# Performance work log

Hardware: AMD Instinct MI355X
Metric: run time of the kernel (lower is better)

## Reference

```python
import jax, jax.numpy as jnp
import numpy as np

B_SI = 4.1491   # neutron scattering length Si (fm)
B_O = 5.803     # neutron scattering length O (fm)
CUTOFF = 3.5    # tetrahedral neighbour cutoff (A)
BIG = 1e6       # masked-distance sentinel (finite to keep grads NaN-free)


def setup_inputs() -> dict:
    key = jax.random.key(0)
    k1, k2 = jax.random.split(key)
    N, L = 4096, 40.0
    positions = jax.random.uniform(k1, (N, 3), dtype=jnp.float32) * L
    cell = (L * jnp.eye(3)).astype(jnp.float32)
    r_bins = (0.05 + 0.05 * jnp.arange(200, dtype=jnp.float32))      # 0.05..10.0 A
    q_bins = jnp.linspace(0.5, 25.0, 500, dtype=jnp.float32)          # A^-1
    species = jax.random.randint(k2, (N,), 0, 3, dtype=jnp.int32)     # 0=Si, 1/2=O
    return {"positions": positions, "cell": cell, "r_bins": r_bins,
            "q_bins": q_bins, "species": species}


def _pair_geometry(positions, cell):
    # Minimum-image displacements under a general periodic cell.
    disp = positions[:, None, :] - positions[None, :, :]        # [N,N,3]
    frac = disp @ jnp.linalg.inv(cell)
    frac = frac - jnp.round(frac)
    disp = frac @ cell
    d2 = jnp.sum(disp * disp, axis=-1)                           # [N,N]
    self_mask = jnp.eye(positions.shape[0], dtype=bool)
    dist = jnp.sqrt(jnp.where(self_mask, 1.0, d2))               # safe sqrt on diag
    return disp, dist, self_mask


def reference(positions, cell, r_bins, q_bins, species):
    N = positions.shape[0]
    nbins = r_bins.shape[0]
    dtype = positions.dtype

    disp, dist, self_mask = _pair_geometry(positions, cell)

    # --- neutron-weighted G(r): differentiable linear (cloud-in-cell) binning ---
    b = jnp.where(species == 0, B_SI, B_O).astype(dtype)         # per-atom scattering length
    w = (b[:, None] * b[None, :]) / (jnp.mean(b) ** 2)           # Faber-Ziman pair weights
    r0, dr = r_bins[0], r_bins[1] - r_bins[0]
    x = (dist - r0) / dr
    i0 = jnp.floor(x).astype(jnp.int32)
    f = x - i0.astype(dtype)
    valid = (~self_mask) & (i0 >= 0) & (i0 < nbins - 1)
    w0 = jnp.where(valid, w * (1.0 - f), 0.0).ravel()
    w1 = jnp.where(valid, w * f, 0.0).ravel()
    i0f = jnp.clip(i0, 0, nbins - 1).ravel()
    hist = (jnp.zeros(nbins, dtype)
            .at[i0f].add(w0)
            .at[jnp.clip(i0f + 1, 0, nbins - 1)].add(w1))
    V = jnp.abs(jnp.linalg.det(cell))
    rho = N / V
    shell = 4.0 * jnp.pi * r_bins ** 2 * dr                       # ideal-gas shell volume
    G_r = hist / (N * rho * shell)                                # [nbins]

    # --- total correlation function T(r) = 4 pi rho r G(r) ---
    T_r = 4.0 * jnp.pi * rho * r_bins * G_r

    # --- structure factor S(Q) = 1 + 4 pi rho int r^2 (G(r)-1) sinc(Qr) dr ---
    qr = q_bins[:, None] * r_bins[None, :]                        # [nQ, nr]
    integrand = (r_bins ** 2) * (G_r - 1.0)
    S_Q = 1.0 + 4.0 * jnp.pi * rho * dr * jnp.sum(
        integrand[None, :] * jnp.sinc(qr / jnp.pi), axis=1)

    # --- tetrahedral order parameter q_tet over Si centres with O neighbours ---
    central = species == 0
    nbr_ok = (species != 0)[None, :] & (~self_mask)
    nd = jnp.where(nbr_ok, dist, BIG)
    negd, idx = jax.lax.top_k(-nd, 4)                             # 4 nearest O per atom
    d4 = -negd                                                    # [N,4]
    u = jnp.take_along_axis(disp, idx[:, :, None], axis=1) / d4[:, :, None]  # unit vecs
    cosang = jnp.einsum('nkd,nld->nkl', u, u)                     # [N,4,4]
    pair_mask = jnp.triu(jnp.ones((4, 4), bool), 1)               # 6 angle pairs
    q_i = 1.0 - (3.0 / 8.0) * jnp.sum(((cosang + 1.0 / 3.0) ** 2) * pair_mask, axis=(1, 2))
    vf = (central & (d4[:, 3] < CUTOFF)).astype(dtype)            # needs 4 nbrs in cutoff
    q_tet = jnp.sum(q_i * vf) / jnp.maximum(jnp.sum(vf), 1.0)

    return G_r, T_r, S_Q, q_tet
```

## Files before the change

kernel.cpp:

```cpp
#include <hip/hip_runtime.h>
#include <climits>
#include <math.h>


#define B_SI_F 4.1491f
#define B_O_F  5.803f
#define CUTOFF_F 3.5f
#define CS2 12.25350025f
#define NCOPIES 16
#define CAP 32

#define WS_HIST 16
#define WS_CNT  4096

__device__ __forceinline__ bool dless(float da, int ia, float db, int ib) {
    return (da < db) || (da == db && ia < ib);
}

struct CellK {
    float ci0, ci1, ci2, ci3, ci4, ci5, ci6, ci7, ci8;
    float c0, c1, c2, c3, c4, c5, c6, c7, c8;
};

__device__ __forceinline__ CellK make_cell(const float* __restrict__ cellm,
                                           bool& diag) {
    CellK K;
    K.c0 = cellm[0]; K.c1 = cellm[1]; K.c2 = cellm[2];
    K.c3 = cellm[3]; K.c4 = cellm[4]; K.c5 = cellm[5];
    K.c6 = cellm[6]; K.c7 = cellm[7]; K.c8 = cellm[8];
    double m0 = K.c0, m1 = K.c1, m2 = K.c2;
    double m3 = K.c3, m4 = K.c4, m5 = K.c5;
    double m6 = K.c6, m7 = K.c7, m8 = K.c8;
    double det = m0*(m4*m8 - m5*m7) - m1*(m3*m8 - m5*m6) + m2*(m3*m7 - m4*m6);
    double rd = 1.0 / det;
    K.ci0 = (float)( (m4*m8 - m5*m7) * rd);
    K.ci1 = (float)(-(m1*m8 - m2*m7) * rd);
    K.ci2 = (float)( (m1*m5 - m2*m4) * rd);
    K.ci3 = (float)(-(m3*m8 - m5*m6) * rd);
    K.ci4 = (float)( (m0*m8 - m2*m6) * rd);
    K.ci5 = (float)(-(m0*m5 - m2*m3) * rd);
    K.ci6 = (float)( (m3*m7 - m4*m6) * rd);
    K.ci7 = (float)(-(m0*m7 - m1*m6) * rd);
    K.ci8 = (float)( (m0*m4 - m1*m3) * rd);
    diag = (K.c1 == 0.0f) && (K.c2 == 0.0f) && (K.c3 == 0.0f) &&
           (K.c5 == 0.0f) && (K.c6 == 0.0f) && (K.c7 == 0.0f);
    return K;
}

template<bool DIAG>
__device__ __forceinline__ void min_image(const CellK& K,
                                          float dx, float dy, float dz,
                                          float& ex, float& ey, float& ez) {
    if (DIAG) {
        float t0 = dx * K.ci0, t1 = dy * K.ci4, t2 = dz * K.ci8;
        t0 -= rintf(t0);  t1 -= rintf(t1);  t2 -= rintf(t2);
        ex = t0 * K.c0;  ey = t1 * K.c4;  ez = t2 * K.c8;
    } else {
        float f0 = dx*K.ci0 + dy*K.ci3 + dz*K.ci6;
        float f1 = dx*K.ci1 + dy*K.ci4 + dz*K.ci7;
        float f2 = dx*K.ci2 + dy*K.ci5 + dz*K.ci8;
        f0 -= rintf(f0);  f1 -= rintf(f1);  f2 -= rintf(f2);
        ex = f0*K.c0 + f1*K.c3 + f2*K.c6;
        ey = f0*K.c1 + f1*K.c4 + f2*K.c7;
        ez = f0*K.c2 + f1*K.c5 + f2*K.c8;
    }
}

template<bool DIAG>
__device__ __forceinline__ void hist_sweep(const CellK& K,
                                           const float4* __restrict__ sj,
                                           const float4* __restrict__ sjc,
                                           int lbase, int jb0,
                                           float fi0, float fi1, float fi2,
                                           float xi, float yi, float zi,
                                           float wi, float inv_dr, float nrb0,
                                           int nbins_m1, float* shc,
                                           bool iSi, bool iO, bool offdiag, int iidx,
                                           float* __restrict__ cnt,
                                           float4* __restrict__ cand) {
    #pragma unroll 4
    for (int l = 0; l < 64; ++l) {
        const float4 pj = sj[lbase + l];
        float d0 = fi0 - pj.x;  d0 -= rintf(d0);
        float d1 = fi1 - pj.y;  d1 -= rintf(d1);
        float d2 = fi2 - pj.z;  d2 -= rintf(d2);
        float ex, ey, ez;
        if (DIAG) {
            ex = d0 * K.c0;  ey = d1 * K.c4;  ez = d2 * K.c8;
        } else {
            ex = d0*K.c0 + d1*K.c3 + d2*K.c6;
            ey = d0*K.c1 + d1*K.c4 + d2*K.c7;
            ez = d0*K.c2 + d1*K.c5 + d2*K.c8;
        }
        float dsq  = fmaf(ex, ex, fmaf(ey, ey, ez * ez));
        float dist = __builtin_amdgcn_sqrtf(dsq);
        float x  = fmaf(dist, inv_dr, nrb0);
        float fl = floorf(x);
        int   i0 = (int)fl;
        if ((unsigned)i0 < (unsigned)nbins_m1) {
            float w  = wi * pj.w;
            float wf = w * (x - fl);
            atomicAdd(&shc[i0],     w - wf);
            atomicAdd(&shc[i0 + 1], wf);
        }
        if (dsq < CS2) {
            const int jg = jb0 + lbase + l;
            if (iSi && pj.w == B_O_F) {
                float old = atomicAdd(&cnt[iidx], 1.0f);
                int slot = (int)rintf(old);
                if (slot < CAP) {
                    float4 cj = sjc[lbase + l];
                    cj.w = __int_as_float(jg);
                    cand[iidx * CAP + slot] = cj;
                }
            }
            if (offdiag && iO && pj.w == B_SI_F) {
                float old = atomicAdd(&cnt[jg], 1.0f);
                int slot = (int)rintf(old);
                if (slot < CAP)
                    cand[jg * CAP + slot] = make_float4(xi, yi, zi, __int_as_float(iidx));
            }
        }
    }
}

__global__ __launch_bounds__(256) void k_main(const float* __restrict__ cellm,
                                              const float* __restrict__ pos,
                                              const int* __restrict__ species,
                                              const float* __restrict__ rbins,
                                              float* __restrict__ ws,
                                              int N, int nbins, int T) {
    const int tid = threadIdx.x;
    const int bid = blockIdx.x;

    bool diag;
    const CellK K = make_cell(cellm, diag);

    __shared__ float sh[4 * 257];
    __shared__ float sjf[128 * 4];
    __shared__ float sjc[128 * 4];

    for (int u = tid; u < 4 * 257; u += 256) sh[u] = 0.0f;

    int rem = bid, ti = 0;
    while (rem >= T - ti) { rem -= T - ti; ti++; }
    const int tj  = ti + rem;
    const int jb0 = tj * 128;

    for (int u = tid; u < 384; u += 256) {
        int g = 3 * jb0 + u;
        sjc[(u / 3) * 4 + (u % 3)] = (g < 3 * N) ? pos[g] : 0.0f;
    }
    if (tid < 128) {
        int ja = jb0 + tid;
        sjf[tid * 4 + 3] = (ja < N) ? ((species[ja] == 0) ? B_SI_F : B_O_F) : 0.0f;
    }
    __syncthreads();
    if (tid < 128) {
        float x = sjc[tid*4], y = sjc[tid*4+1], z = sjc[tid*4+2];
        float f0, f1, f2;
        if (diag) { f0 = x*K.ci0; f1 = y*K.ci4; f2 = z*K.ci8; }
        else {
            f0 = x*K.ci0 + y*K.ci3 + z*K.ci6;
            f1 = x*K.ci1 + y*K.ci4 + z*K.ci7;
            f2 = x*K.ci2 + y*K.ci5 + z*K.ci8;
        }
        sjf[tid*4] = f0;  sjf[tid*4+1] = f1;  sjf[tid*4+2] = f2;
    }

    const float rb0      = rbins[0];
    const float inv_dr   = 1.0f / (rbins[1] - rbins[0]);
    const float nrb0     = -rb0 * inv_dr;
    const int   nbins_m1 = nbins - 1;

    const int il  = tid & 127;
    const int sub = tid >> 7;
    const int i   = ti * 128 + il;
    const int ig  = min(i, N - 1);
    const float xi = pos[3*ig], yi = pos[3*ig+1], zi = pos[3*ig+2];
    float fi0, fi1, fi2;
    if (diag) { fi0 = xi*K.ci0; fi1 = yi*K.ci4; fi2 = zi*K.ci8; }
    else {
        fi0 = xi*K.ci0 + yi*K.ci3 + zi*K.ci6;
        fi1 = xi*K.ci1 + yi*K.ci4 + zi*K.ci7;
        fi2 = xi*K.ci2 + yi*K.ci5 + zi*K.ci8;
    }
    const int   spi  = species[ig];
    const float b_i  = (spi == 0) ? B_SI_F : B_O_F;
    const float wmul = (ti == tj) ? 1.0f : 2.0f;
    const float wi   = (i < N) ? b_i * wmul : 0.0f;
    const bool iSi = (i < N) && (spi == 0);
    const bool iO  = (i < N) && (spi != 0);
    const bool offdiag = (ti != tj);

    float*  cnt  = ws + WS_CNT;
    float4* cand = (float4*)(ws + WS_CNT + 3 * (size_t)N);
    float*  shc  = sh + ((tid >> 4) & 3) * 257;

    __syncthreads();

    const float4* sj  = (const float4*)sjf;
    const float4* sjc4 = (const float4*)sjc;
    const int lbase = sub * 64;
    if (diag) hist_sweep<true >(K, sj, sjc4, lbase, jb0, fi0, fi1, fi2, xi, yi, zi, wi, inv_dr, nrb0, nbins_m1, shc, iSi, iO, offdiag, i, cnt, cand);
    else      hist_sweep<false>(K, sj, sjc4, lbase, jb0, fi0, fi1, fi2, xi, yi, zi, wi, inv_dr, nrb0, nbins_m1, shc, iSi, iO, offdiag, i, cnt, cand);

    __syncthreads();

    float* gh = ws + WS_HIST + (size_t)(bid % NCOPIES) * nbins;
    for (int t = tid; t < nbins; t += 256) {
        float h = sh[t] + sh[257 + t] + sh[514 + t] + sh[771 + t];
        if (h != 0.0f) atomicAdd(&gh[t], h);
    }
}

#define INS4D(c, jc, ex, ey, ez)                                           \
{                                                                          \
    if (dless(c, jc, e3, j3)) {                                            \
        bool lt2 = dless(c, jc, e2, j2);                                   \
        bool lt1 = dless(c, jc, e1, j1);                                   \
        bool lt0 = dless(c, jc, e0, j0);                                   \
        e3 = lt2 ? e2 : c;               j3 = lt2 ? j2 : jc;               \
        x3 = lt2 ? x2 : ex;  y3 = lt2 ? y2 : ey;  z3 = lt2 ? z2 : ez;      \
        e2 = lt2 ? (lt1 ? e1 : c) : e2;  j2 = lt2 ? (lt1 ? j1 : jc) : j2;  \
        x2 = lt2 ? (lt1 ? x1 : ex) : x2;                                   \
        y2 = lt2 ? (lt1 ? y1 : ey) : y2;                                   \
        z2 = lt2 ? (lt1 ? z1 : ez) : z2;                                   \
        e1 = lt1 ? (lt0 ? e0 : c) : e1;  j1 = lt1 ? (lt0 ? j0 : jc) : j1;  \
        x1 = lt1 ? (lt0 ? x0 : ex) : x1;                                   \
        y1 = lt1 ? (lt0 ? y0 : ey) : y1;                                   \
        z1 = lt1 ? (lt0 ? z0 : ez) : z1;                                   \
        e0 = lt0 ? c : e0;               j0 = lt0 ? jc : j0;               \
        x0 = lt0 ? ex : x0;  y0 = lt0 ? ey : y0;  z0 = lt0 ? ez : z0;      \
    }                                                                      \
}

__global__ __launch_bounds__(256) void k_tet(const float* __restrict__ cellm,
                                             const float* __restrict__ pos,
                                             const int* __restrict__ species,
                                             float* __restrict__ ws, int N) {
    const int s = __builtin_amdgcn_readfirstlane(blockIdx.x * 4 + (threadIdx.x >> 6));
    if (s >= N) return;
    const int lane = threadIdx.x & 63;

    float* cnt = ws + WS_CNT;
    float* qv  = ws + WS_CNT + N;
    const float4* cand = (const float4*)(ws + WS_CNT + 3 * (size_t)N);

    if (species[s] != 0) {
        if (lane == 0) { qv[2*s] = 0.0f; qv[2*s + 1] = 0.0f; }
        return;
    }

    bool diag;
    const CellK K = make_cell(cellm, diag);
    const float xi = pos[3*s], yi = pos[3*s+1], zi = pos[3*s+2];

    const int c = (int)rintf(cnt[s]);
    if (lane == 0) cnt[s] = 0.0f;

    float e0 = 1e30f, e1 = 1e30f, e2 = 1e30f, e3 = 1e30f;
    int   j0 = INT_MAX, j1 = INT_MAX, j2 = INT_MAX, j3 = INT_MAX;
    float x0 = 0, y0 = 0, z0 = 0, x1 = 0, y1 = 0, z1 = 0;
    float x2 = 0, y2 = 0, z2 = 0, x3 = 0, y3 = 0, z3 = 0;

    if (c <= CAP) {
        if (lane < c) {
            float4 cd = cand[s * CAP + lane];
            int j = __float_as_int(cd.w);
            float ex, ey, ez;
            if (diag) min_image<true >(K, xi - cd.x, yi - cd.y, zi - cd.z, ex, ey, ez);
            else      min_image<false>(K, xi - cd.x, yi - cd.y, zi - cd.z, ex, ey, ez);
            e0 = fmaf(ex, ex, fmaf(ey, ey, ez * ez));
            j0 = j;  x0 = ex;  y0 = ey;  z0 = ez;
        }
    } else {
        for (int k = lane; k < N; k += 64) {
            int   sp = species[k];
            float px = pos[3*k], py = pos[3*k+1], pz = pos[3*k+2];
            float ex, ey, ez;
            if (diag) min_image<true >(K, xi - px, yi - py, zi - pz, ex, ey, ez);
            else      min_image<false>(K, xi - px, yi - py, zi - pz, ex, ey, ez);
            float d2 = fmaf(ex, ex, fmaf(ey, ey, ez * ez));
            float cc = (sp != 0 && k != s) ? d2 : 1e30f;
            int   jc = k;
            INS4D(cc, jc, ex, ey, ez)
        }
    }

    float r0d, r1d, r2d, r3d;
    int   r0j, r1j, r2j, r3j;
    float rx[4], ry[4], rz[4];
    #define EXTRACT_MIN(RD, RJ, RK)                                    \
    {                                                                  \
        float md = e0; int mj = j0;                                    \
        float mx = x0, my = y0, mz = z0;                               \
        for (int off = 32; off > 0; off >>= 1) {                       \
            float od = __shfl_xor(md, off, 64);                        \
            int   oj = __shfl_xor(mj, off, 64);                        \
            float ox = __shfl_xor(mx, off, 64);                        \
            float oy = __shfl_xor(my, off, 64);                        \
            float oz = __shfl_xor(mz, off, 64);                        \
            bool keep = dless(md, mj, od, oj);                         \
            md = keep ? md : od;  mj = keep ? mj : oj;                 \
            mx = keep ? mx : ox;  my = keep ? my : oy;                 \
            mz = keep ? mz : oz;                                       \
        }                                                              \
        RD = md; RJ = mj; rx[RK] = mx; ry[RK] = my; rz[RK] = mz;       \
        bool pop = (j0 == mj);                                         \
        e0 = pop ? e1 : e0;  j0 = pop ? j1 : j0;                       \
        x0 = pop ? x1 : x0;  y0 = pop ? y1 : y0;  z0 = pop ? z1 : z0;  \
        e1 = pop ? e2 : e1;  j1 = pop ? j2 : j1;                       \
        x1 = pop ? x2 : x1;  y1 = pop ? y2 : y1;  z1 = pop ? z2 : z1;  \
        e2 = pop ? e3 : e2;  j2 = pop ? j3 : j2;                       \
        x2 = pop ? x3 : x2;  y2 = pop ? y3 : y2;  z2 = pop ? z3 : z2;  \
        e3 = pop ? 1e30f : e3;  j3 = pop ? INT_MAX : j3;               \
    }
    EXTRACT_MIN(r0d, r0j, 0)
    EXTRACT_MIN(r1d, r1j, 1)
    EXTRACT_MIN(r2d, r2j, 2)
    EXTRACT_MIN(r3d, r3j, 3)
    #undef EXTRACT_MIN

    if (lane == 0) {
        float qiv = 0.0f, vf = 0.0f;
        if (r3j != INT_MAX) {
            float dd[4] = {sqrtf(r0d), sqrtf(r1d), sqrtf(r2d), sqrtf(r3d)};
            if (dd[3] < CUTOFF_F) {
                float ux[4], uy[4], uz[4];
                #pragma unroll
                for (int k = 0; k < 4; ++k) {
                    ux[k] = rx[k] / dd[k];
                    uy[k] = ry[k] / dd[k];
                    uz[k] = rz[k] / dd[k];
                }
                float s2 = 0.0f;
                #pragma unroll
                for (int k = 0; k < 4; ++k)
                    #pragma unroll
                    for (int l = k + 1; l < 4; ++l) {
                        float cs = ux[k]*ux[l] + uy[k]*uy[l] + uz[k]*uz[l];
                        float t  = cs + (1.0f / 3.0f);
                        s2 += t * t;
                    }
                qiv = 1.0f - 0.375f * s2;
                vf  = 1.0f;
            }
        }
        qv[2*s]     = qiv;
        qv[2*s + 1] = vf;
    }
}

__device__ __forceinline__ float fast_sinc(float x) {
    float rev = x * 0.15915494309189535f;
    rev -= rintf(rev);
    float sn = __builtin_amdgcn_sinf(rev);
    return sn * __builtin_amdgcn_rcpf(x);
}

__global__ __launch_bounds__(256) void k_fin(const float* __restrict__ cellm,
                                             const float* __restrict__ ws,
                                             const float* __restrict__ rbins,
                                             const float* __restrict__ qbins,
                                             const int* __restrict__ species,
                                             float* __restrict__ out,
                                             int N, int nbins, int nq) {
    __shared__ float2 srw[256];
    __shared__ float rq[256], rv[256];
    __shared__ int   scnt[256];
    const int tid = threadIdx.x;

    double m0 = cellm[0], m1 = cellm[1], m2 = cellm[2];
    double m3 = cellm[3], m4 = cellm[4], m5 = cellm[5];
    double m6 = cellm[6], m7 = cellm[7], m8 = cellm[8];
    double det = m0*(m4*m8 - m5*m7) - m1*(m3*m8 - m5*m6) + m2*(m3*m7 - m4*m6);
    const float rho = (float)((double)N / fabs(det));

    {
        int c = 0;
        for (int k = tid; k < N; k += 256) c += (species[k] == 0) ? 1 : 0;
        scnt[tid] = c;
    }
    __syncthreads();
    for (int s = 128; s > 0; s >>= 1) {
        if (tid < s) scnt[tid] += scnt[tid + s];
        __syncthreads();
    }
    const int nSi = scnt[0];
    const float mean_b  = ((float)nSi * B_SI_F + (float)(N - nSi) * B_O_F) / (float)N;
    const float w_scale = 1.0f / (mean_b * mean_b);

    const float dr = rbins[1] - rbins[0];
    const float FOURPI = 4.0f * 3.14159265358979323846f;

    for (int t = tid; t < nbins; t += blockDim.x) {
        float h = 0.0f;
        #pragma unroll
        for (int c = 0; c < NCOPIES; ++c) h += ws[WS_HIST + c * nbins + t];
        h *= w_scale;
        float r = rbins[t];
        float shell = FOURPI * r * r * dr;
        float g = h / ((float)N * rho * shell);
        srw[t] = make_float2(r, r * r * (g - 1.0f));
        if (blockIdx.x == 0) {
            out[t] = g;
            out[nbins + t] = FOURPI * rho * r * g;
        }
    }

    if (blockIdx.x == 0) {
        const float* qv = ws + WS_CNT + N;
        float sq = 0.0f, sv = 0.0f;
        for (int s = tid; s < N; s += 256) {
            sq += qv[2*s];
            sv += qv[2*s + 1];
        }
        rq[tid] = sq; rv[tid] = sv;
    }
    __syncthreads();
    if (blockIdx.x == 0) {
        for (int s = 128; s > 0; s >>= 1) {
            if (tid < s) { rq[tid] += rq[tid + s]; rv[tid] += rv[tid + s]; }
            __syncthreads();
        }
        if (tid == 0)
            out[2 * nbins + nq] = rq[0] / fmaxf(rv[0], 1.0f);
    }

    int q = blockIdx.x * blockDim.x + tid;
    if (q < nq) {
        float qq = qbins[q];
        float s0 = 0.0f, s1 = 0.0f, s2 = 0.0f, s3 = 0.0f;
        int t = 0;
        for (; t + 4 <= nbins; t += 4) {
            float2 a = srw[t], b = srw[t+1], c = srw[t+2], d = srw[t+3];
            s0 += a.y * fast_sinc(qq * a.x);
            s1 += b.y * fast_sinc(qq * b.x);
            s2 += c.y * fast_sinc(qq * c.x);
            s3 += d.y * fast_sinc(qq * d.x);
        }
        for (; t < nbins; ++t) {
            float2 a = srw[t];
            s0 += a.y * fast_sinc(qq * a.x);
        }
        float s = (s0 + s1) + (s2 + s3);
        out[2 * nbins + q] = 1.0f + FOURPI * rho * dr * s;
    }
}

extern "C" void kernel_launch(void* const* d_in, const int* in_sizes, int n_in,
                              void* d_out, int out_size, void* d_ws, size_t ws_size,
                              hipStream_t stream) {
    const float* pos     = (const float*)d_in[0];
    const float* cell    = (const float*)d_in[1];
    const float* rbins   = (const float*)d_in[2];
    const float* qbins   = (const float*)d_in[3];
    const int*   species = (const int*)d_in[4];
    float* out = (float*)d_out;
    float* ws  = (float*)d_ws;

    const int N     = in_sizes[4];
    const int nbins = in_sizes[2];
    const int nq    = in_sizes[3];

    const int T  = (N + 127) / 128;
    const int P  = T * (T + 1) / 2;
    const int BT = (N + 3) / 4;
    const int QB = (nq + 255) / 256;

    k_main<<<P, 256, 0, stream>>>(cell, pos, species, rbins, ws, N, nbins, T);
    k_tet<<<BT, 256, 0, stream>>>(cell, pos, species, ws, N);
    k_fin<<<QB, 256, 0, stream>>>(cell, ws, rbins, qbins, species, out, N, nbins, nq);
}
```

Before: 101.2 us.

## Fuse tetrahedral order kernel into final S(Q) kernel with atomic reduction

Removes the separate k_tet launch and runs its per-Si-atom work as extra blocks appended to the k_fin grid. The per-atom q/valid array and block 0's serial reduction over it are replaced by per-block atomic adds into 64 striped accumulators, with a last-block-done counter finishing q_tet. The intent is to save one kernel launch and gap, and to overlap the tetrahedral work with the sinc transform. The accumulators and the done counter are never reset in the code shown, so correctness depends on the workspace being cleared before each call.

```diff
diff --git a/kernel.cpp b/kernel.cpp
--- a/kernel.cpp
+++ b/kernel.cpp
@@ -11,6 +11,7 @@
 #define CAP 32
 
 #define WS_HIST 16
+#define WS_ACC  3328
 #define WS_CNT  4096
 
 __device__ __forceinline__ bool dless(float da, int ia, float db, int ib) {
@@ -194,12 +195,12 @@
     const bool offdiag = (ti != tj);
 
     float*  cnt  = ws + WS_CNT;
-    float4* cand = (float4*)(ws + WS_CNT + 3 * (size_t)N);
+    float4* cand = (float4*)(ws + WS_CNT + (size_t)N);
     float*  shc  = sh + ((tid >> 4) & 3) * 257;
 
     __syncthreads();
 
-    const float4* sj  = (const float4*)sjf;
+    const float4* sj   = (const float4*)sjf;
     const float4* sjc4 = (const float4*)sjc;
     const int lbase = sub * 64;
     if (diag) hist_sweep<true >(K, sj, sjc4, lbase, jb0, fi0, fi1, fi2, xi, yi, zi, wi, inv_dr, nrb0, nbins_m1, shc, iSi, iO, offdiag, i, cnt, cand);
@@ -235,123 +236,6 @@
     }                                                                      \
 }
 
-__global__ __launch_bounds__(256) void k_tet(const float* __restrict__ cellm,
-                                             const float* __restrict__ pos,
-                                             const int* __restrict__ species,
-                                             float* __restrict__ ws, int N) {
-    const int s = __builtin_amdgcn_readfirstlane(blockIdx.x * 4 + (threadIdx.x >> 6));
-    if (s >= N) return;
-    const int lane = threadIdx.x & 63;
-
-    float* cnt = ws + WS_CNT;
-    float* qv  = ws + WS_CNT + N;
-    const float4* cand = (const float4*)(ws + WS_CNT + 3 * (size_t)N);
-
-    if (species[s] != 0) {
-        if (lane == 0) { qv[2*s] = 0.0f; qv[2*s + 1] = 0.0f; }
-        return;
-    }
-
-    bool diag;
-    const CellK K = make_cell(cellm, diag);
-    const float xi = pos[3*s], yi = pos[3*s+1], zi = pos[3*s+2];
-
-    const int c = (int)rintf(cnt[s]);
-    if (lane == 0) cnt[s] = 0.0f;
-
-    float e0 = 1e30f, e1 = 1e30f, e2 = 1e30f, e3 = 1e30f;
-    int   j0 = INT_MAX, j1 = INT_MAX, j2 = INT_MAX, j3 = INT_MAX;
-    float x0 = 0, y0 = 0, z0 = 0, x1 = 0, y1 = 0, z1 = 0;
-    float x2 = 0, y2 = 0, z2 = 0, x3 = 0, y3 = 0, z3 = 0;
-
-    if (c <= CAP) {
-        if (lane < c) {
-            float4 cd = cand[s * CAP + lane];
-            int j = __float_as_int(cd.w);
-            float ex, ey, ez;
-            if (diag) min_image<true >(K, xi - cd.x, yi - cd.y, zi - cd.z, ex, ey, ez);
-            else      min_image<false>(K, xi - cd.x, yi - cd.y, zi - cd.z, ex, ey, ez);
-            e0 = fmaf(ex, ex, fmaf(ey, ey, ez * ez));
-            j0 = j;  x0 = ex;  y0 = ey;  z0 = ez;
-        }
-    } else {
-        for (int k = lane; k < N; k += 64) {
-            int   sp = species[k];
-            float px = pos[3*k], py = pos[3*k+1], pz = pos[3*k+2];
-            float ex, ey, ez;
-            if (diag) min_image<true >(K, xi - px, yi - py, zi - pz, ex, ey, ez);
-            else      min_image<false>(K, xi - px, yi - py, zi - pz, ex, ey, ez);
-            float d2 = fmaf(ex, ex, fmaf(ey, ey, ez * ez));
-            float cc = (sp != 0 && k != s) ? d2 : 1e30f;
-            int   jc = k;
-            INS4D(cc, jc, ex, ey, ez)
-        }
-    }
-
-    float r0d, r1d, r2d, r3d;
-    int   r0j, r1j, r2j, r3j;
-    float rx[4], ry[4], rz[4];
-    #define EXTRACT_MIN(RD, RJ, RK)                                    \
-    {                                                                  \
-        float md = e0; int mj = j0;                                    \
-        float mx = x0, my = y0, mz = z0;                               \
-        for (int off = 32; off > 0; off >>= 1) {                       \
-            float od = __shfl_xor(md, off, 64);                        \
-            int   oj = __shfl_xor(mj, off, 64);                        \
-            float ox = __shfl_xor(mx, off, 64);                        \
-            float oy = __shfl_xor(my, off, 64);                        \
-            float oz = __shfl_xor(mz, off, 64);                        \
-            bool keep = dless(md, mj, od, oj);                         \
-            md = keep ? md : od;  mj = keep ? mj : oj;                 \
-            mx = keep ? mx : ox;  my = keep ? my : oy;                 \
-            mz = keep ? mz : oz;                                       \
-        }                                                              \
-        RD = md; RJ = mj; rx[RK] = mx; ry[RK] = my; rz[RK] = mz;       \
-        bool pop = (j0 == mj);                                         \
-        e0 = pop ? e1 : e0;  j0 = pop ? j1 : j0;                       \
-        x0 = pop ? x1 : x0;  y0 = pop ? y1 : y0;  z0 = pop ? z1 : z0;  \
-        e1 = pop ? e2 : e1;  j1 = pop ? j2 : j1;                       \
-        x1 = pop ? x2 : x1;  y1 = pop ? y2 : y1;  z1 = pop ? z2 : z1;  \
-        e2 = pop ? e3 : e2;  j2 = pop ? j3 : j2;                       \
-        x2 = pop ? x3 : x2;  y2 = pop ? y3 : y2;  z2 = pop ? z3 : z2;  \
-        e3 = pop ? 1e30f : e3;  j3 = pop ? INT_MAX : j3;               \
-    }
-    EXTRACT_MIN(r0d, r0j, 0)
-    EXTRACT_MIN(r1d, r1j, 1)
-    EXTRACT_MIN(r2d, r2j, 2)
-    EXTRACT_MIN(r3d, r3j, 3)
-    #undef EXTRACT_MIN
-
-    if (lane == 0) {
-        float qiv = 0.0f, vf = 0.0f;
-        if (r3j != INT_MAX) {
-            float dd[4] = {sqrtf(r0d), sqrtf(r1d), sqrtf(r2d), sqrtf(r3d)};
-            if (dd[3] < CUTOFF_F) {
-                float ux[4], uy[4], uz[4];
-                #pragma unroll
-                for (int k = 0; k < 4; ++k) {
-                    ux[k] = rx[k] / dd[k];
-                    uy[k] = ry[k] / dd[k];
-                    uz[k] = rz[k] / dd[k];
-                }
-                float s2 = 0.0f;
-                #pragma unroll
-                for (int k = 0; k < 4; ++k)
-                    #pragma unroll
-                    for (int l = k + 1; l < 4; ++l) {
-                        float cs = ux[k]*ux[l] + uy[k]*uy[l] + uz[k]*uz[l];
-                        float t  = cs + (1.0f / 3.0f);
-                        s2 += t * t;
-                    }
-                qiv = 1.0f - 0.375f * s2;
-                vf  = 1.0f;
-            }
-        }
-        qv[2*s]     = qiv;
-        qv[2*s + 1] = vf;
-    }
-}
-
 __device__ __forceinline__ float fast_sinc(float x) {
     float rev = x * 0.15915494309189535f;
     rev -= rintf(rev);
@@ -360,16 +244,150 @@
 }
 
 __global__ __launch_bounds__(256) void k_fin(const float* __restrict__ cellm,
-                                             const float* __restrict__ ws,
+                                             float* __restrict__ ws,
                                              const float* __restrict__ rbins,
                                              const float* __restrict__ qbins,
                                              const int* __restrict__ species,
+                                             const float* __restrict__ pos,
                                              float* __restrict__ out,
-                                             int N, int nbins, int nq) {
+                                             int N, int nbins, int nq,
+                                             int QB, int BT) {
+    const int tid = threadIdx.x;
+    const int bid = blockIdx.x;
+
+    if (bid >= QB) {
+        __shared__ float swq[4], swv[4];
+        __shared__ float sacc[128];
+        __shared__ int   slast;
+        const int tb   = bid - QB;
+        const int wid  = tid >> 6;
+        const int lane = tid & 63;
+        const int s = __builtin_amdgcn_readfirstlane(tb * 4 + wid);
+
+        float* cnt = ws + WS_CNT;
+        const float4* cand = (const float4*)(ws + WS_CNT + (size_t)N);
+
+        float qiv = 0.0f, vf = 0.0f;
+        if (s < N && species[s] == 0) {
+            bool diag;
+            const CellK K = make_cell(cellm, diag);
+            const float xi = pos[3*s], yi = pos[3*s+1], zi = pos[3*s+2];
+            const int c = (int)rintf(cnt[s]);
+            if (lane == 0) cnt[s] = 0.0f;
+
+            float e0 = 1e30f, e1 = 1e30f, e2 = 1e30f, e3 = 1e30f;
+            int   j0 = INT_MAX, j1 = INT_MAX, j2 = INT_MAX, j3 = INT_MAX;
+            float x0 = 0, y0 = 0, z0 = 0, x1 = 0, y1 = 0, z1 = 0;
+            float x2 = 0, y2 = 0, z2 = 0, x3 = 0, y3 = 0, z3 = 0;
+
+            if (c <= CAP) {
+                if (lane < c) {
+                    float4 cd = cand[s * CAP + lane];
+                    int j = __float_as_int(cd.w);
+                    float ex, ey, ez;
+                    if (diag) min_image<true >(K, xi - cd.x, yi - cd.y, zi - cd.z, ex, ey, ez);
+                    else      min_image<false>(K, xi - cd.x, yi - cd.y, zi - cd.z, ex, ey, ez);
+                    e0 = fmaf(ex, ex, fmaf(ey, ey, ez * ez));
+                    j0 = j;  x0 = ex;  y0 = ey;  z0 = ez;
+                }
+            } else {
+                for (int k = lane; k < N; k += 64) {
+                    int   sp = species[k];
+                    float px = pos[3*k], py = pos[3*k+1], pz = pos[3*k+2];
+                    float ex, ey, ez;
+                    if (diag) min_image<true >(K, xi - px, yi - py, zi - pz, ex, ey, ez);
+                    else      min_image<false>(K, xi - px, yi - py, zi - pz, ex, ey, ez);
+                    float d2 = fmaf(ex, ex, fmaf(ey, ey, ez * ez));
+                    float cc = (sp != 0 && k != s) ? d2 : 1e30f;
+                    int   jc = k;
+                    INS4D(cc, jc, ex, ey, ez)
+                }
+            }
+
+            float r0d, r1d, r2d, r3d;
+            int   r0j, r1j, r2j, r3j;
+            float rx[4], ry[4], rz[4];
+            #define EXTRACT_MIN(RD, RJ, RK)                                    \
+            {                                                                  \
+                float md = e0; int mj = j0;                                    \
+                float mx = x0, my = y0, mz = z0;                               \
+                for (int off = 32; off > 0; off >>= 1) {                       \
+                    float od = __shfl_xor(md, off, 64);                        \
+                    int   oj = __shfl_xor(mj, off, 64);                        \
+                    float ox = __shfl_xor(mx, off, 64);                        \
+                    float oy = __shfl_xor(my, off, 64);                        \
+                    float oz = __shfl_xor(mz, off, 64);                        \
+                    bool keep = dless(md, mj, od, oj);                         \
+                    md = keep ? md : od;  mj = keep ? mj : oj;                 \
+                    mx = keep ? mx : ox;  my = keep ? my : oy;                 \
+                    mz = keep ? mz : oz;                                       \
+                }                                                              \
+                RD = md; RJ = mj; rx[RK] = mx; ry[RK] = my; rz[RK] = mz;       \
+                bool pop = (j0 == mj);                                         \
+                e0 = pop ? e1 : e0;  j0 = pop ? j1 : j0;                       \
+                x0 = pop ? x1 : x0;  y0 = pop ? y1 : y0;  z0 = pop ? z1 : z0;  \
+                e1 = pop ? e2 : e1;  j1 = pop ? j2 : j1;                       \
+                x1 = pop ? x2 : x1;  y1 = pop ? y2 : y1;  z1 = pop ? z2 : z1;  \
+                e2 = pop ? e3 : e2;  j2 = pop ? j3 : j2;                       \
+                x2 = pop ? x3 : x2;  y2 = pop ? y3 : y2;  z2 = pop ? z3 : z2;  \
+                e3 = pop ? 1e30f : e3;  j3 = pop ? INT_MAX : j3;               \
+            }
+            EXTRACT_MIN(r0d, r0j, 0)
+            EXTRACT_MIN(r1d, r1j, 1)
+            EXTRACT_MIN(r2d, r2j, 2)
+            EXTRACT_MIN(r3d, r3j, 3)
+            #undef EXTRACT_MIN
+
+            if (lane == 0 && r3j != INT_MAX) {
+                float dd[4] = {sqrtf(r0d), sqrtf(r1d), sqrtf(r2d), sqrtf(r3d)};
+                if (dd[3] < CUTOFF_F) {
+                    float ux[4], uy[4], uz[4];
+                    #pragma unroll
+                    for (int k = 0; k < 4; ++k) {
+                        ux[k] = rx[k] / dd[k];
+                        uy[k] = ry[k] / dd[k];
+                        uz[k] = rz[k] / dd[k];
+                    }
+                    float s2 = 0.0f;
+                    #pragma unroll
+                    for (int k = 0; k < 4; ++k)
+                        #pragma unroll
+                        for (int l = k + 1; l < 4; ++l) {
+                            float cs = ux[k]*ux[l] + uy[k]*uy[l] + uz[k]*uz[l];
+                            float t  = cs + (1.0f / 3.0f);
+                            s2 += t * t;
+                        }
+                    qiv = 1.0f - 0.375f * s2;
+                    vf  = 1.0f;
+                }
+            }
+        }
+        if (lane == 0) { swq[wid] = qiv; swv[wid] = vf; }
+        __syncthreads();
+        if (tid == 0) {
+            float bsq = swq[0] + swq[1] + swq[2] + swq[3];
+            float bsv = swv[0] + swv[1] + swv[2] + swv[3];
+            atomicAdd(&ws[WS_ACC + (tb & 63)], bsq);
+            atomicAdd(&ws[WS_ACC + 64 + (tb & 63)], bsv);
+            asm volatile("s_waitcnt vmcnt(0)" ::: "memory");
+            float old = atomicAdd(&ws[WS_ACC + 128], 1.0f);
+            slast = (old > (float)BT - 1.5f) ? 1 : 0;
+        }
+        __syncthreads();
+        if (slast) {
+            if (tid < 128) sacc[tid] = atomicAdd(&ws[WS_ACC + tid], 0.0f);
+            __syncthreads();
+            if (tid == 0) {
+                float tq = 0.0f, tv = 0.0f;
+                for (int k = 0; k < 64; ++k) { tq += sacc[k]; tv += sacc[64 + k]; }
+                out[2 * nbins + nq] = tq / fmaxf(tv, 1.0f);
+            }
+        }
+        return;
+    }
+
     __shared__ float2 srw[256];
-    __shared__ float rq[256], rv[256];
-    __shared__ int   scnt[256];
-    const int tid = threadIdx.x;
+    __shared__ int    scnt[256];
 
     double m0 = cellm[0], m1 = cellm[1], m2 = cellm[2];
     double m3 = cellm[3], m4 = cellm[4], m5 = cellm[5];
@@ -403,32 +421,14 @@
         float shell = FOURPI * r * r * dr;
         float g = h / ((float)N * rho * shell);
         srw[t] = make_float2(r, r * r * (g - 1.0f));
-        if (blockIdx.x == 0) {
+        if (bid == 0) {
             out[t] = g;
             out[nbins + t] = FOURPI * rho * r * g;
         }
     }
-
-    if (blockIdx.x == 0) {
-        const float* qv = ws + WS_CNT + N;
-        float sq = 0.0f, sv = 0.0f;
-        for (int s = tid; s < N; s += 256) {
-            sq += qv[2*s];
-            sv += qv[2*s + 1];
-        }
-        rq[tid] = sq; rv[tid] = sv;
-    }
     __syncthreads();
-    if (blockIdx.x == 0) {
-        for (int s = 128; s > 0; s >>= 1) {
-            if (tid < s) { rq[tid] += rq[tid + s]; rv[tid] += rv[tid + s]; }
-            __syncthreads();
-        }
-        if (tid == 0)
-            out[2 * nbins + nq] = rq[0] / fmaxf(rv[0], 1.0f);
-    }
-
-    int q = blockIdx.x * blockDim.x + tid;
+
+    int q = bid * blockDim.x + tid;
     if (q < nq) {
         float qq = qbins[q];
         float s0 = 0.0f, s1 = 0.0f, s2 = 0.0f, s3 = 0.0f;
@@ -470,6 +470,5 @@
     const int QB = (nq + 255) / 256;
 
     k_main<<<P, 256, 0, stream>>>(cell, pos, species, rbins, ws, N, nbins, T);
-    k_tet<<<BT, 256, 0, stream>>>(cell, pos, species, ws, N);
-    k_fin<<<QB, 256, 0, stream>>>(cell, ws, rbins, qbins, species, out, N, nbins, nq);
-}
+    k_fin<<<QB + BT, 256, 0, stream>>>(cell, ws, rbins, qbins, species, pos, out, N, nbins, nq, QB, BT);
+}
```

Result: faster. 97.71 us (-3.4%).
